# Performance work log

Hardware: AMD Instinct MI355X
Metric: run time of the kernel (lower is better)

The kernel has to match this reference:

```python
import jax, jax.numpy as jnp
import numpy as np

PROBE = 1.0
ALPHA = 0.5


def setup_inputs() -> dict:
    key = jax.random.key(0)
    ks = jax.random.split(key, 8)
    B, L, D = 4096, 128, 64  # batch, n_cats (fields), d_embed
    NG, NL = 2, 2
    cat_indices = jax.random.randint(ks[0], (B, L), 0, L, dtype=jnp.int64)
    emb_table = jax.random.normal(ks[1], (L, D), dtype=jnp.float32)
    acc_w = jax.random.normal(ks[2], (D, D), dtype=jnp.float32) * (1.0 / np.sqrt(D))
    acc_b = jnp.zeros((D,), dtype=jnp.float32)
    gw = jax.random.normal(ks[3], (NG, D, D), dtype=jnp.float32) * (1.0 / np.sqrt(D))
    gb = jnp.zeros((NG, D), dtype=jnp.float32)
    lw = jax.random.normal(ks[4], (NL, D, D), dtype=jnp.float32) * (1.0 / np.sqrt(D))
    lb = jnp.zeros((NL, D), dtype=jnp.float32)
    return {"cat_indices": cat_indices, "emb_table": emb_table, "acc_w": acc_w,
            "acc_b": acc_b, "gw": gw, "gb": gb, "lw": lw, "lb": lb}


def reference(cat_indices, emb_table, acc_w, acc_b, gw, gb, lw, lb):
    B, L = cat_indices.shape
    # shallow embedding lookup: [B, L, D]
    emb = emb_table[cat_indices]
    # uniform + probe*I adjacency, row-normalized by (L + probe); identical per sample
    adj = (jnp.ones((L, L), emb.dtype) + PROBE * jnp.eye(L, dtype=emb.dtype)) / (L + PROBE)
    # global branch: adj @ (emb @ W) + b
    support = jnp.einsum('bld,de->ble', emb, acc_w)
    g = jnp.einsum('lm,bme->ble', adj, support) + acc_b
    g = jax.nn.relu(g)
    n_global = gw.shape[0]
    for i in range(n_global):
        g = jnp.einsum('bld,ed->ble', g, gw[i]) + gb[i]
        if i + 1 < n_global:
            g = jax.nn.relu(g)
    # local FM branch: 0.5 * ((sum e)^2 - sum e^2)  -> [B, D]
    s = jnp.sum(emb, axis=1)
    loc = 0.5 * (s * s - jnp.sum(emb * emb, axis=1))
    n_local = lw.shape[0]
    for i in range(n_local):
        loc = loc @ lw[i].T + lb[i]
        if i + 1 < n_local:
            loc = jax.nn.relu(loc)
    # broadcast local [B, D] against global [B, L, D]
    return ALPHA * g + (1.0 - ALPHA) * loc[:, None, :]
```

## Files before the change

### kernel.cpp

```cpp
#include <hip/hip_runtime.h>
#include <hip/hip_bf16.h>


typedef __attribute__((ext_vector_type(8))) short bf16x8;
typedef __attribute__((ext_vector_type(4))) float f32x4;
typedef __attribute__((ext_vector_type(2))) unsigned int u32x2;

#define RECIP129 (1.0f/129.0f)

static __device__ __forceinline__ unsigned int cvt_pk_bf16(float lo, float hi){
  unsigned int r;
  asm("v_cvt_pk_bf16_f32 %0, %1, %2" : "=v"(r) : "v"(lo), "v"(hi));
  return r;
}
static __device__ __forceinline__ bf16x8 pack8(const float* v){
  uint4 p;
  p.x = cvt_pk_bf16(v[0], v[1]); p.y = cvt_pk_bf16(v[2], v[3]);
  p.z = cvt_pk_bf16(v[4], v[5]); p.w = cvt_pk_bf16(v[6], v[7]);
  return __builtin_bit_cast(bf16x8, p);
}

__global__ __launch_bounds__(256) void combined_kernel(
    const int*   __restrict__ cat,
    const float* __restrict__ emb,
    const float* __restrict__ acc_w,
    const float* __restrict__ acc_b,
    const float* __restrict__ lw,
    const float* __restrict__ lb,
    const float* __restrict__ gw,
    const float* __restrict__ gbias,
    unsigned int* __restrict__ tsupb,
    uint4* __restrict__ fragtab,
    float* __restrict__ u_pg,
    float* __restrict__ loc2g)
{
  const int tid = threadIdx.x;
  const int blk = blockIdx.x;

  if (blk >= 256){
    if (blk < 264){
      int local = blk - 256;
      int k = local*16 + (tid >> 4), e0 = (tid & 15)*4;
      float a0=0.f, a1=0.f, a2=0.f, a3=0.f;
      for (int d = 0; d < 64; ++d){
        float ev = emb[k*64 + d];
        float4 wv = *reinterpret_cast<const float4*>(acc_w + d*64 + e0);
        a0 += ev*wv.x; a1 += ev*wv.y; a2 += ev*wv.z; a3 += ev*wv.w;
      }
      tsupb[k*32 + (e0 >> 1)]     = cvt_pk_bf16(a0*RECIP129, a1*RECIP129);
      tsupb[k*32 + (e0 >> 1) + 1] = cvt_pk_bf16(a2*RECIP129, a3*RECIP129);
    } else {
      int lane = tid & 63, r = lane & 15, h = lane >> 4;
      #pragma unroll
      for (int i = 0; i < 4; ++i){
        int f = (tid >> 6) + i*4;
        int layer = f >> 3, nt = (f >> 1) & 3, kc = f & 1;
        float sc = layer ? 0.5f : 1.0f;
        const float* p0 = gw + layer*4096 + (nt*16 + r)*64 + kc*32 + h*8;
        float4 a = *reinterpret_cast<const float4*>(p0);
        float4 c = *reinterpret_cast<const float4*>(p0 + 4);
        uint4 v;
        v.x = cvt_pk_bf16(sc*a.x, sc*a.y); v.y = cvt_pk_bf16(sc*a.z, sc*a.w);
        v.z = cvt_pk_bf16(sc*c.x, sc*c.y); v.w = cvt_pk_bf16(sc*c.z, sc*c.w);
        fragtab[f*64 + lane] = v;
      }
    }
    return;
  }

  __shared__ int hist[16*128];
  __shared__ __align__(16) unsigned int cbf[16*64];
  __shared__ __align__(16) unsigned short srows[16*64];
  __shared__ __align__(16) unsigned short lrows[16*64];
  const int w = tid >> 6, lane = tid & 63;
  const int r = lane & 15, h = lane >> 4;
  const int bbase = blk * 16;
  const int n = w*16 + h*4;
  const unsigned int swzr = (unsigned)(r & 7) << 4;

  #pragma unroll
  for (int i = 0; i < 8; ++i) hist[tid*8 + i] = 0;

  bf16x8 af_s[4], af_q[4], aw[2], l0f[2], l1f[2];
  {
    float vs[8], vq[8];
    #pragma unroll
    for (int kc = 0; kc < 4; ++kc){
      #pragma unroll
      for (int j = 0; j < 8; ++j){
        float x = emb[(kc*32 + h*8 + j)*64 + w*16 + r];
        vs[j] = x; vq[j] = x*x;
      }
      af_s[kc] = pack8(vs);
      af_q[kc] = pack8(vq);
    }
    #pragma unroll
    for (int kc = 0; kc < 2; ++kc){
      #pragma unroll
      for (int j = 0; j < 8; ++j)
        vs[j] = acc_w[(kc*32 + h*8 + j)*64 + w*16 + r] * RECIP129;
      aw[kc] = pack8(vs);
      const float* p0 = lw + (w*16 + r)*64 + kc*32 + h*8;
      float4 a = *reinterpret_cast<const float4*>(p0);
      float4 c = *reinterpret_cast<const float4*>(p0 + 4);
      float t0[8] = {a.x,a.y,a.z,a.w,c.x,c.y,c.z,c.w};
      l0f[kc] = pack8(t0);
      a = *reinterpret_cast<const float4*>(p0 + 4096);
      c = *reinterpret_cast<const float4*>(p0 + 4100);
      float t1[8] = {a.x,a.y,a.z,a.w,c.x,c.y,c.z,c.w};
      l1f[kc] = pack8(t1);
    }
  }
  float accb[4], lb0v[4], bias05[4];
  #pragma unroll
  for (int reg = 0; reg < 4; ++reg){
    accb[reg]   = acc_b[n + reg];
    lb0v[reg]   = lb[n + reg];
    bias05[reg] = 0.5f*(lb[64 + n + reg] + gbias[64 + n + reg]);
  }

  __syncthreads();
  {
    int b_l = tid >> 4, l0 = (tid & 15) * 8;
    const int* cp = cat + (bbase + b_l)*128 + l0;
    int4 i0 = *reinterpret_cast<const int4*>(cp);
    int4 i1 = *reinterpret_cast<const int4*>(cp + 4);
    atomicAdd(&hist[b_l*128 + i0.x], 1); atomicAdd(&hist[b_l*128 + i0.y], 1);
    atomicAdd(&hist[b_l*128 + i0.z], 1); atomicAdd(&hist[b_l*128 + i0.w], 1);
    atomicAdd(&hist[b_l*128 + i1.x], 1); atomicAdd(&hist[b_l*128 + i1.y], 1);
    atomicAdd(&hist[b_l*128 + i1.z], 1); atomicAdd(&hist[b_l*128 + i1.w], 1);
  }
  __syncthreads();
  {
    int b_l = tid >> 4, c0 = (tid & 15) * 8;
    float f[8];
    #pragma unroll
    for (int i = 0; i < 8; ++i) f[i] = (float)hist[b_l*128 + c0 + i];
    uint4 v;
    v.x = cvt_pk_bf16(f[0], f[1]); v.y = cvt_pk_bf16(f[2], f[3]);
    v.z = cvt_pk_bf16(f[4], f[5]); v.w = cvt_pk_bf16(f[6], f[7]);
    *reinterpret_cast<uint4*>((char*)cbf + b_l*256 + ((unsigned)(c0*2) ^ ((unsigned)(b_l & 7) << 4))) = v;
  }
  __syncthreads();

  const char* crow = (const char*)cbf + r*256;
  f32x4 acc_s = {0,0,0,0}, acc_q = {0,0,0,0};
  #pragma unroll
  for (int kc = 0; kc < 4; ++kc){
    bf16x8 cf = __builtin_bit_cast(bf16x8,
        *reinterpret_cast<const uint4*>(crow + ((unsigned)(kc*64 + h*16) ^ swzr)));
    acc_s = __builtin_amdgcn_mfma_f32_16x16x32_bf16(af_s[kc], cf, acc_s, 0, 0, 0);
    acc_q = __builtin_amdgcn_mfma_f32_16x16x32_bf16(af_q[kc], cf, acc_q, 0, 0, 0);
  }

  char* srow = (char*)srows + r*128;
  char* lrow = (char*)lrows + r*128;
  const unsigned int off = ((unsigned)(w*32 + h*8)) ^ swzr;
  {
    u32x2 ps, pl;
    ps[0] = cvt_pk_bf16(acc_s[0], acc_s[1]);
    ps[1] = cvt_pk_bf16(acc_s[2], acc_s[3]);
    float l0 = 0.5f*(acc_s[0]*acc_s[0] - acc_q[0]);
    float l1 = 0.5f*(acc_s[1]*acc_s[1] - acc_q[1]);
    float l2v = 0.5f*(acc_s[2]*acc_s[2] - acc_q[2]);
    float l3 = 0.5f*(acc_s[3]*acc_s[3] - acc_q[3]);
    pl[0] = cvt_pk_bf16(l0, l1); pl[1] = cvt_pk_bf16(l2v, l3);
    *reinterpret_cast<u32x2*>(srow + off) = ps;
    *reinterpret_cast<u32x2*>(lrow + off) = pl;
  }
  __syncthreads();

  f32x4 acc_u; acc_u[0]=accb[0]; acc_u[1]=accb[1]; acc_u[2]=accb[2]; acc_u[3]=accb[3];
  f32x4 acc_h = {0,0,0,0};
  #pragma unroll
  for (int kc = 0; kc < 2; ++kc){
    unsigned o = ((unsigned)(kc*64 + h*16)) ^ swzr;
    bf16x8 sb = __builtin_bit_cast(bf16x8, *reinterpret_cast<const uint4*>((char*)srows + r*128 + o));
    bf16x8 lf = __builtin_bit_cast(bf16x8, *reinterpret_cast<const uint4*>((char*)lrows + r*128 + o));
    acc_u = __builtin_amdgcn_mfma_f32_16x16x32_bf16(aw[kc],  sb, acc_u, 0, 0, 0);
    acc_h = __builtin_amdgcn_mfma_f32_16x16x32_bf16(l0f[kc], lf, acc_h, 0, 0, 0);
  }
  {
    float4 st; st.x = acc_u[0]; st.y = acc_u[1]; st.z = acc_u[2]; st.w = acc_u[3];
    *reinterpret_cast<float4*>(u_pg + (size_t)(bbase + r)*64 + n) = st;
  }
  __syncthreads();
  {
    u32x2 ph;
    ph[0] = cvt_pk_bf16(fmaxf(acc_h[0] + lb0v[0], 0.f), fmaxf(acc_h[1] + lb0v[1], 0.f));
    ph[1] = cvt_pk_bf16(fmaxf(acc_h[2] + lb0v[2], 0.f), fmaxf(acc_h[3] + lb0v[3], 0.f));
    *reinterpret_cast<u32x2*>(lrow + off) = ph;
  }
  __syncthreads();

  f32x4 acc2 = {0,0,0,0};
  #pragma unroll
  for (int kc = 0; kc < 2; ++kc){
    unsigned o = ((unsigned)(kc*64 + h*16)) ^ swzr;
    bf16x8 hf = __builtin_bit_cast(bf16x8, *reinterpret_cast<const uint4*>((char*)lrows + r*128 + o));
    acc2 = __builtin_amdgcn_mfma_f32_16x16x32_bf16(l1f[kc], hf, acc2, 0, 0, 0);
  }
  {
    float4 st;
    st.x = 0.5f*acc2[0] + bias05[0]; st.y = 0.5f*acc2[1] + bias05[1];
    st.z = 0.5f*acc2[2] + bias05[2]; st.w = 0.5f*acc2[3] + bias05[3];
    *reinterpret_cast<float4*>(loc2g + (size_t)(bbase + r)*64 + n) = st;
  }
}

__global__ __launch_bounds__(256) void fused_kernel(
    const int*          __restrict__ cat,
    const unsigned int* __restrict__ tsupb,
    const float*        __restrict__ u_pg,
    const float*        __restrict__ loc2g,
    const uint4*        __restrict__ fragtab,
    const float*        __restrict__ gbias,
    float*              __restrict__ out)
{
  __shared__ __align__(16) unsigned short ts[128*72];
  __shared__ __align__(16) unsigned short gbuf[4][16*64];

  const int tid = threadIdx.x, wid = tid >> 6, lane = tid & 63;
  const int b = blockIdx.x*4 + wid;
  const int r = lane & 15, h = lane >> 4;

  {
    int k = tid >> 1, half = tid & 1;
    const uint4* src = reinterpret_cast<const uint4*>(tsupb) + k*8 + half*4;
    char* rowp = (char*)&ts[k*72];
    unsigned int swz = (unsigned)(k & 3) << 4;
    #pragma unroll
    for (int i = 0; i < 4; ++i)
      *reinterpret_cast<uint4*>(rowp + ((unsigned)(half*64 + i*16) ^ swz)) = src[i];
  }

  int k0 = cat[b*128 + lane];
  int k1 = cat[b*128 + 64 + lane];

  float uf[16];
  #pragma unroll
  for (int kc = 0; kc < 2; ++kc){
    const float* up = u_pg + (size_t)b*64 + kc*32 + h*8;
    float4 a = *reinterpret_cast<const float4*>(up);
    float4 c = *reinterpret_cast<const float4*>(up + 4);
    uf[kc*8+0]=a.x; uf[kc*8+1]=a.y; uf[kc*8+2]=a.z; uf[kc*8+3]=a.w;
    uf[kc*8+4]=c.x; uf[kc*8+5]=c.y; uf[kc*8+6]=c.z; uf[kc*8+7]=c.w;
  }
  f32x4 c2i[4], gb0f[4];
  #pragma unroll
  for (int mt = 0; mt < 4; ++mt){
    float4 lv = *reinterpret_cast<const float4*>(loc2g + (size_t)b*64 + mt*16 + h*4);
    f32x4 t; t[0]=lv.x; t[1]=lv.y; t[2]=lv.z; t[3]=lv.w;
    c2i[mt] = t;
    float4 gv = *reinterpret_cast<const float4*>(gbias + mt*16 + h*4);
    f32x4 g; g[0]=gv.x; g[1]=gv.y; g[2]=gv.z; g[3]=gv.w;
    gb0f[mt] = g;
  }
  bf16x8 w0[4][2], w1[4][2];
  #pragma unroll
  for (int nt = 0; nt < 4; ++nt)
    #pragma unroll
    for (int kc = 0; kc < 2; ++kc){
      w0[nt][kc] = __builtin_bit_cast(bf16x8, fragtab[(nt*2 + kc)*64 + lane]);
      w1[nt][kc] = __builtin_bit_cast(bf16x8, fragtab[(8 + nt*2 + kc)*64 + lane]);
    }

  __syncthreads();

  char* myrowW = (char*)&gbuf[wid][0] + r*128;
  const unsigned int rsw8 = (unsigned)(r & 7) << 4;

  for (int tl = 0; tl < 8; ++tl){
    const int rowbase = b*128 + tl*16;
    int kk = __shfl(tl < 4 ? k0 : k1, (tl & 3)*16 + r);

    const char* trow = (const char*)&ts[kk*72];
    const unsigned int ksw = (unsigned)(kk & 3) << 4;
    bf16x8 a0[2];
    #pragma unroll
    for (int kc = 0; kc < 2; ++kc){
      uint4 wv = *reinterpret_cast<const uint4*>(trow + ((unsigned)(kc*64 + h*16) ^ ksw));
      unsigned int ow[4];
      const unsigned int* wp = &wv.x;
      #pragma unroll
      for (int q = 0; q < 4; ++q){
        unsigned int wq = wp[q];
        float lo = fmaxf(__uint_as_float(wq << 16)         + uf[kc*8 + 2*q],     0.f);
        float hi = fmaxf(__uint_as_float(wq & 0xffff0000u) + uf[kc*8 + 2*q + 1], 0.f);
        ow[q] = cvt_pk_bf16(lo, hi);
      }
      uint4 packed; packed.x=ow[0]; packed.y=ow[1]; packed.z=ow[2]; packed.w=ow[3];
      a0[kc] = __builtin_bit_cast(bf16x8, packed);
    }

    f32x4 acc1[4];
    #pragma unroll
    for (int nt = 0; nt < 4; ++nt) acc1[nt] = gb0f[nt];
    #pragma unroll
    for (int kc = 0; kc < 2; ++kc)
      #pragma unroll
      for (int nt = 0; nt < 4; ++nt)
        acc1[nt] = __builtin_amdgcn_mfma_f32_16x16x32_bf16(w0[nt][kc], a0[kc], acc1[nt], 0, 0, 0);

    #pragma unroll
    for (int nt = 0; nt < 4; ++nt){
      u32x2 p;
      p[0] = cvt_pk_bf16(fmaxf(acc1[nt][0], 0.f), fmaxf(acc1[nt][1], 0.f));
      p[1] = cvt_pk_bf16(fmaxf(acc1[nt][2], 0.f), fmaxf(acc1[nt][3], 0.f));
      *reinterpret_cast<u32x2*>(myrowW + ((unsigned)(nt*32 + h*8) ^ rsw8)) = p;
    }

    bf16x8 a1[2];
    #pragma unroll
    for (int kc = 0; kc < 2; ++kc)
      a1[kc] = __builtin_bit_cast(bf16x8,
                 *reinterpret_cast<const uint4*>(myrowW + ((unsigned)(kc*64 + h*16) ^ rsw8)));

    f32x4 acc2[4];
    #pragma unroll
    for (int mt = 0; mt < 4; ++mt) acc2[mt] = c2i[mt];
    #pragma unroll
    for (int kc = 0; kc < 2; ++kc)
      #pragma unroll
      for (int mt = 0; mt < 4; ++mt)
        acc2[mt] = __builtin_amdgcn_mfma_f32_16x16x32_bf16(w1[mt][kc], a1[kc], acc2[mt], 0, 0, 0);

    float* orow = out + (size_t)(rowbase + r)*64 + h*4;
    #pragma unroll
    for (int mt = 0; mt < 4; ++mt){
      float4 st;
      st.x = acc2[mt][0]; st.y = acc2[mt][1];
      st.z = acc2[mt][2]; st.w = acc2[mt][3];
      *reinterpret_cast<float4*>(orow + mt*16) = st;
    }
  }
}

extern "C" void kernel_launch(void* const* d_in, const int* in_sizes, int n_in,
                              void* d_out, int out_size, void* d_ws, size_t ws_size,
                              hipStream_t stream) {
  const int*   cat   = (const int*)  d_in[0];
  const float* emb   = (const float*)d_in[1];
  const float* acc_w = (const float*)d_in[2];
  const float* acc_b = (const float*)d_in[3];
  const float* gw    = (const float*)d_in[4];
  const float* gb    = (const float*)d_in[5];
  const float* lw    = (const float*)d_in[6];
  const float* lb    = (const float*)d_in[7];
  float* out = (float*)d_out;

  const int B = in_sizes[0] / 128;

  float* ws           = (float*)d_ws;
  unsigned int* tsupb = (unsigned int*)ws;
  uint4* fragtab      = (uint4*)(ws + 4096);
  float* u_pg         = ws + 8192;
  float* loc2g        = u_pg + (size_t)B*64;

  hipLaunchKernelGGL(combined_kernel, dim3(265), dim3(256), 0, stream,
                     cat, emb, acc_w, acc_b, lw, lb, gw, gb,
                     tsupb, fragtab, u_pg, loc2g);
  hipLaunchKernelGGL(fused_kernel, dim3(B/4), dim3(256), 0, stream,
                     cat, tsupb, u_pg, loc2g, fragtab, gb, out);
}
```

Before: 35.90 us.

## Drop LDS staging of support table and reload weight fragments per tile

Removes the per-block copy of the 128x64 bf16 support table into shared memory, along with the block-wide barrier; rows are now gathered straight from global memory (expected to sit in L1/L2). The weight fragments are no longer held in registers across the loop but reloaded from global memory inside each MFMA loop. Launch bounds now request higher occupancy. The aim is to cut LDS footprint, register pressure and block startup cost, at the price of more global and cache loads on every tile iteration.

```diff
diff --git a/kernel.cpp b/kernel.cpp
--- a/kernel.cpp
+++ b/kernel.cpp
@@ -208,7 +208,7 @@
   }
 }
 
-__global__ __launch_bounds__(256) void fused_kernel(
+__global__ __launch_bounds__(256, 4) void fused_kernel(
     const int*          __restrict__ cat,
     const unsigned int* __restrict__ tsupb,
     const float*        __restrict__ u_pg,
@@ -217,22 +217,11 @@
     const float*        __restrict__ gbias,
     float*              __restrict__ out)
 {
-  __shared__ __align__(16) unsigned short ts[128*72];
   __shared__ __align__(16) unsigned short gbuf[4][16*64];
 
   const int tid = threadIdx.x, wid = tid >> 6, lane = tid & 63;
   const int b = blockIdx.x*4 + wid;
   const int r = lane & 15, h = lane >> 4;
-
-  {
-    int k = tid >> 1, half = tid & 1;
-    const uint4* src = reinterpret_cast<const uint4*>(tsupb) + k*8 + half*4;
-    char* rowp = (char*)&ts[k*72];
-    unsigned int swz = (unsigned)(k & 3) << 4;
-    #pragma unroll
-    for (int i = 0; i < 4; ++i)
-      *reinterpret_cast<uint4*>(rowp + ((unsigned)(half*64 + i*16) ^ swz)) = src[i];
-  }
 
   int k0 = cat[b*128 + lane];
   int k1 = cat[b*128 + 64 + lane];
@@ -256,16 +245,6 @@
     f32x4 g; g[0]=gv.x; g[1]=gv.y; g[2]=gv.z; g[3]=gv.w;
     gb0f[mt] = g;
   }
-  bf16x8 w0[4][2], w1[4][2];
-  #pragma unroll
-  for (int nt = 0; nt < 4; ++nt)
-    #pragma unroll
-    for (int kc = 0; kc < 2; ++kc){
-      w0[nt][kc] = __builtin_bit_cast(bf16x8, fragtab[(nt*2 + kc)*64 + lane]);
-      w1[nt][kc] = __builtin_bit_cast(bf16x8, fragtab[(8 + nt*2 + kc)*64 + lane]);
-    }
-
-  __syncthreads();
 
   char* myrowW = (char*)&gbuf[wid][0] + r*128;
   const unsigned int rsw8 = (unsigned)(r & 7) << 4;
@@ -274,12 +253,11 @@
     const int rowbase = b*128 + tl*16;
     int kk = __shfl(tl < 4 ? k0 : k1, (tl & 3)*16 + r);
 
-    const char* trow = (const char*)&ts[kk*72];
-    const unsigned int ksw = (unsigned)(kk & 3) << 4;
+    const uint4* trow = reinterpret_cast<const uint4*>(tsupb + kk*32);
     bf16x8 a0[2];
     #pragma unroll
     for (int kc = 0; kc < 2; ++kc){
-      uint4 wv = *reinterpret_cast<const uint4*>(trow + ((unsigned)(kc*64 + h*16) ^ ksw));
+      uint4 wv = trow[kc*4 + h];
       unsigned int ow[4];
       const unsigned int* wp = &wv.x;
       #pragma unroll
@@ -299,8 +277,10 @@
     #pragma unroll
     for (int kc = 0; kc < 2; ++kc)
       #pragma unroll
-      for (int nt = 0; nt < 4; ++nt)
-        acc1[nt] = __builtin_amdgcn_mfma_f32_16x16x32_bf16(w0[nt][kc], a0[kc], acc1[nt], 0, 0, 0);
+      for (int nt = 0; nt < 4; ++nt){
+        bf16x8 w0f = __builtin_bit_cast(bf16x8, fragtab[(nt*2 + kc)*64 + lane]);
+        acc1[nt] = __builtin_amdgcn_mfma_f32_16x16x32_bf16(w0f, a0[kc], acc1[nt], 0, 0, 0);
+      }
 
     #pragma unroll
     for (int nt = 0; nt < 4; ++nt){
@@ -322,8 +302,10 @@
     #pragma unroll
     for (int kc = 0; kc < 2; ++kc)
       #pragma unroll
-      for (int mt = 0; mt < 4; ++mt)
-        acc2[mt] = __builtin_amdgcn_mfma_f32_16x16x32_bf16(w1[mt][kc], a1[kc], acc2[mt], 0, 0, 0);
+      for (int mt = 0; mt < 4; ++mt){
+        bf16x8 w1f = __builtin_bit_cast(bf16x8, fragtab[(8 + mt*2 + kc)*64 + lane]);
+        acc2[mt] = __builtin_amdgcn_mfma_f32_16x16x32_bf16(w1f, a1[kc], acc2[mt], 0, 0, 0);
+      }
 
     float* orow = out + (size_t)(rowbase + r)*64 + h*4;
     #pragma unroll
```

Measured after the change: 51.91 us. 1.45x slower.
